# Kernel tuning notes

Measured on AMD Instinct MI355X. Metric: run time of the kernel, lower is better.

The kernel has to match this reference:

```python
import jax, jax.numpy as jnp
import numpy as np

N_NODES = 100000


def _gcn_conv(x, edge_index, W, b, num_nodes):
    """PyG GCNConv: x' = D^{-1/2} (A + I) D^{-1/2} (x W) + b."""
    xl = x @ W  # [N, H]
    loop = jnp.arange(num_nodes)
    row = jnp.concatenate([edge_index[0], loop])  # source
    col = jnp.concatenate([edge_index[1], loop])  # target
    deg = jax.ops.segment_sum(jnp.ones_like(col, dtype=xl.dtype), col,
                              num_segments=num_nodes)
    dinv = jnp.where(deg > 0, jax.lax.rsqrt(deg), 0.0)
    norm = dinv[row] * dinv[col]  # [E + N]
    msgs = xl[row] * norm[:, None]  # gather + scale
    out = jax.ops.segment_sum(msgs, col, num_segments=num_nodes)
    return out + b


def setup_inputs() -> dict:
    key = jax.random.key(0)
    ks = jax.random.split(key, 6)
    N, E, D, H, O = N_NODES, 1600000, 128, 64, 1
    x = jax.random.normal(ks[0], (N, D), dtype=jnp.float32)
    edge_index = jax.random.randint(ks[1], (2, E), 0, N, dtype=jnp.int64)
    W1 = jax.random.normal(ks[2], (D, H), dtype=jnp.float32) / np.sqrt(D)
    b1 = jnp.zeros((H,), dtype=jnp.float32)
    W2 = jax.random.normal(ks[3], (H, H), dtype=jnp.float32) / np.sqrt(H)
    b2 = jnp.zeros((H,), dtype=jnp.float32)
    Wfc = jax.random.normal(ks[4], (H, O), dtype=jnp.float32) / np.sqrt(H)
    bfc = jnp.zeros((O,), dtype=jnp.float32)
    return {"x": x, "edge_index": edge_index, "W1": W1, "b1": b1,
            "W2": W2, "b2": b2, "Wfc": Wfc, "bfc": bfc}


def reference(x, edge_index, W1, b1, W2, b2, Wfc, bfc):
    N = x.shape[0]
    h = jax.nn.relu(_gcn_conv(x, edge_index, W1, b1, N))
    h = jax.nn.relu(_gcn_conv(h, edge_index, W2, b2, N))
    return jax.nn.sigmoid(h @ Wfc + bfc)  # [N, 1]
```

## Files before the change

kernel.cpp:

```cpp
#include <hip/hip_runtime.h>
#include <math.h>


typedef __attribute__((ext_vector_type(8))) short bf16x8;
typedef __attribute__((ext_vector_type(4))) float f32x4;
typedef __attribute__((ext_vector_type(2))) float f32x2;

#define CHUNKS 1024

__device__ __forceinline__ unsigned short f2bf(float f) {
    unsigned u = __float_as_uint(f);
    u += 0x7FFFu + ((u >> 16) & 1u);
    return (unsigned short)(u >> 16);
}
__device__ __forceinline__ unsigned packbf(float a, float b) {
    return (unsigned)f2bf(a) | ((unsigned)f2bf(b) << 16);
}
__device__ __forceinline__ void upadd2(uint4 g, f32x2* a) {
    a[0] += (f32x2){__uint_as_float(g.x << 16), __uint_as_float(g.x & 0xFFFF0000u)};
    a[1] += (f32x2){__uint_as_float(g.y << 16), __uint_as_float(g.y & 0xFFFF0000u)};
    a[2] += (f32x2){__uint_as_float(g.z << 16), __uint_as_float(g.z & 0xFFFF0000u)};
    a[3] += (f32x2){__uint_as_float(g.w << 16), __uint_as_float(g.w & 0xFFFF0000u)};
}

__global__ __launch_bounds__(256) void k_hist(const int* __restrict__ col, int E,
                                              int NBUK, int CH,
                                              int* __restrict__ hist_g) {
    __shared__ int h[256];
    for (int i = threadIdx.x; i < NBUK; i += 256) h[i] = 0;
    __syncthreads();
    int base = blockIdx.x * CH, hi = min(base + CH, E);
    for (int e = base + (int)threadIdx.x; e < hi; e += 256)
        atomicAdd(&h[col[e] >> 9], 1);
    __syncthreads();
    for (int i = threadIdx.x; i < NBUK; i += 256)
        hist_g[blockIdx.x * NBUK + i] = h[i];
}

__global__ __launch_bounds__(256) void k_colscan(const int* __restrict__ hist_g, int NBUK,
                                                 int* __restrict__ histOff,
                                                 int* __restrict__ bucketTotal) {
    __shared__ int s[256];
    const int b = blockIdx.x, t = threadIdx.x;
    int v[4], sum = 0;
#pragma unroll
    for (int j = 0; j < 4; ++j) {
        v[j] = hist_g[(t * 4 + j) * NBUK + b];
        sum += v[j];
    }
    s[t] = sum;
    __syncthreads();
    for (int off = 1; off < 256; off <<= 1) {
        int u = (t >= off) ? s[t - off] : 0;
        __syncthreads();
        s[t] += u;
        __syncthreads();
    }
    int run = s[t] - sum;
#pragma unroll
    for (int j = 0; j < 4; ++j) {
        histOff[b * CHUNKS + t * 4 + j] = run;
        run += v[j];
    }
    if (t == 255) bucketTotal[b] = run;
}

__global__ __launch_bounds__(256) void k_scan_tot(const int* __restrict__ bucketTotal,
                                                  int NBUK, int E, int N,
                                                  int* __restrict__ bucketBase,
                                                  int* __restrict__ row_off) {
    __shared__ int s[256];
    int t = threadIdx.x;
    int v = (t < NBUK) ? bucketTotal[t] : 0;
    s[t] = v;
    __syncthreads();
    for (int off = 1; off < 256; off <<= 1) {
        int u = (t >= off) ? s[t - off] : 0;
        __syncthreads();
        s[t] += u;
        __syncthreads();
    }
    if (t < NBUK) bucketBase[t] = s[t] - v;
    if (t == 0) row_off[N] = E;
}

__global__ __launch_bounds__(256) void k_scatter(const int* __restrict__ row,
                                                 const int* __restrict__ col, int E,
                                                 int NBUK, int CH,
                                                 const int* __restrict__ bucketBase,
                                                 const int* __restrict__ histOff,
                                                 unsigned* __restrict__ ebuf) {
    __shared__ int cur[256];
    for (int i = threadIdx.x; i < NBUK; i += 256)
        cur[i] = bucketBase[i] + histOff[i * CHUNKS + blockIdx.x];
    __syncthreads();
    int base = blockIdx.x * CH, hi = min(base + CH, E);
    for (int e = base + (int)threadIdx.x; e < hi; e += 256) {
        int d = col[e], src = row[e];
        int b = d >> 9;
        int pos = atomicAdd(&cur[b], 1);
        ebuf[pos] = ((unsigned)(d & 511) << 17) | (unsigned)src;
    }
}

__global__ __launch_bounds__(512) void k_bucket(const unsigned* __restrict__ ebuf,
                                                const int* __restrict__ bucketBase,
                                                const int* __restrict__ bucketTotal,
                                                int N,
                                                int* __restrict__ row_off,
                                                float* __restrict__ dinv,
                                                int* __restrict__ csr_src) {
    __shared__ int hc[512], of[512];
    const int bid = blockIdx.x, t = threadIdx.x;
    const int base = bucketBase[bid];
    const int cnt  = bucketTotal[bid];
    hc[t] = 0;
    __syncthreads();
    for (int i = t; i < cnt; i += 512)
        atomicAdd(&hc[ebuf[base + i] >> 17], 1);
    __syncthreads();
    int v = hc[t];
    of[t] = v;
    __syncthreads();
    for (int off = 1; off < 512; off <<= 1) {
        int u = (t >= off) ? of[t - off] : 0;
        __syncthreads();
        of[t] += u;
        __syncthreads();
    }
    int excl = of[t] - v;
    int node = bid * 512 + t;
    if (node < N) {
        row_off[node] = base + excl;
        dinv[node] = rsqrtf((float)(v + 1));
    }
    of[t] = excl;
    __syncthreads();
    for (int i = t; i < cnt; i += 512) {
        unsigned e = ebuf[base + i];
        int dl = (int)(e >> 17), src = (int)(e & 0x1FFFFu);
        int pos = atomicAdd(&of[dl], 1);
        csr_src[base + pos] = src;
    }
}

template <int K, bool BF16IN>
__global__ __launch_bounds__(256) void k_gemm_mfma(const void* __restrict__ xin,
                                                   const float* __restrict__ W,
                                                   const float* __restrict__ dinv,
                                                   unsigned short* __restrict__ out,
                                                   int N) {
    constexpr int KS = K + 8;
    __shared__ short sX[64 * KS];
    __shared__ short sW[64 * KS];
    const int tid = threadIdx.x;
    const int wv = tid >> 6, lane = tid & 63;
    const int q = lane >> 4, m = lane & 15;
    const int nb = blockIdx.x * 64;

    for (int i = tid; i < K * 64; i += 256) {
        int k = i >> 6, c = i & 63;
        sW[c * KS + k] = (short)f2bf(W[i]);
    }
    if (BF16IN) {
        const unsigned short* xb = (const unsigned short*)xin;
        for (int i = tid; i < 64 * (K / 8); i += 256) {
            int r = i / (K / 8), c8 = (i % (K / 8)) * 8;
            int node = nb + r;
            uint4 v = make_uint4(0u, 0u, 0u, 0u);
            if (node < N) v = *(const uint4*)(xb + (size_t)node * K + c8);
            *(uint4*)(&sX[r * KS + c8]) = v;
        }
    } else {
        const float* xf = (const float*)xin;
        for (int i = tid; i < 64 * (K / 8); i += 256) {
            int r = i / (K / 8), c8 = (i % (K / 8)) * 8;
            int node = nb + r;
            uint4 v = make_uint4(0u, 0u, 0u, 0u);
            if (node < N) {
                float4 lo = *(const float4*)(xf + (size_t)node * K + c8);
                float4 hi = *(const float4*)(xf + (size_t)node * K + c8 + 4);
                v.x = packbf(lo.x, lo.y);
                v.y = packbf(lo.z, lo.w);
                v.z = packbf(hi.x, hi.y);
                v.w = packbf(hi.z, hi.w);
            }
            *(uint4*)(&sX[r * KS + c8]) = v;
        }
    }
    __syncthreads();

    f32x4 acc[4] = {};
    const short* aRow = &sX[(wv * 16 + m) * KS + q * 8];
#pragma unroll
    for (int k0 = 0; k0 < K; k0 += 32) {
        bf16x8 a = *(const bf16x8*)(aRow + k0);
#pragma unroll
        for (int ft = 0; ft < 4; ++ft) {
            bf16x8 b = *(const bf16x8*)(&sW[(ft * 16 + m) * KS + k0 + q * 8]);
            acc[ft] = __builtin_amdgcn_mfma_f32_16x16x32_bf16(a, b, acc[ft], 0, 0, 0);
        }
    }
#pragma unroll
    for (int r = 0; r < 4; ++r) {
        int node = nb + wv * 16 + q * 4 + r;
        if (node < N) {
            float di = dinv[node];
#pragma unroll
            for (int ft = 0; ft < 4; ++ft)
                out[(size_t)node * 64 + ft * 16 + m] = f2bf(acc[ft][r] * di);
        }
    }
}

__global__ __launch_bounds__(256) void k_agg_g2(const unsigned short* __restrict__ xl,
                                                const int* __restrict__ row_off,
                                                const int* __restrict__ csr_src,
                                                const float* __restrict__ dinv,
                                                const float* __restrict__ bias,
                                                const float* __restrict__ W2,
                                                unsigned short* __restrict__ out, int N) {
    constexpr int KS = 72;
    __shared__ short sH[4 * 16 * KS];
    __shared__ short sW2[64 * KS];
    const int tid = threadIdx.x;
    const int wv = tid >> 6, lane = tid & 63;
    const int s = lane >> 3, o = lane & 7;
    const int q = lane >> 4, m = lane & 15;

    for (int i = tid; i < 64 * 64; i += 256) {
        int k = i >> 6, n = i & 63;
        sW2[n * KS + k] = (short)f2bf(W2[i]);
    }
    short* myH = &sH[wv * 16 * KS];
    for (int i = lane; i < 8 * KS / 4; i += 64)
        ((unsigned long long*)(myH + 8 * KS))[i] = 0ull;
    __syncthreads();

    const int base8 = (blockIdx.x * 4 + wv) * 8;
    int node = base8 + s;
    const bool active = node < N;
    node = min(node, N - 1);
    const int beg = row_off[node];
    const int deg = row_off[node + 1] - beg;
    const int cnt = active ? deg + 1 : 0;
    int mx = cnt;
    mx = max(mx, __shfl_xor(mx, 8, 64));
    mx = max(mx, __shfl_xor(mx, 16, 64));
    mx = max(mx, __shfl_xor(mx, 32, 64));
    const char* xlb = (const char*)xl;
    const unsigned loff = (unsigned)(o << 4);
    f32x2 acc0[4] = {}, acc1[4] = {};
    int idx[4];
#pragma unroll
    for (int j = 0; j < 4; ++j) idx[j] = (j < deg) ? csr_src[beg + j] : node;
    for (int it = 0; it < mx; it += 4) {
        int c[4];
        bool v[4];
#pragma unroll
        for (int j = 0; j < 4; ++j) {
            c[j] = idx[j];
            v[j] = (it + j) < cnt;
            idx[j] = (it + 4 + j < deg) ? csr_src[beg + it + 4 + j] : node;
        }
        uint4 g0 = *(const uint4*)(xlb + (((unsigned)c[0] << 7) | loff));
        uint4 g1 = *(const uint4*)(xlb + (((unsigned)c[1] << 7) | loff));
        uint4 g2 = *(const uint4*)(xlb + (((unsigned)c[2] << 7) | loff));
        uint4 g3 = *(const uint4*)(xlb + (((unsigned)c[3] << 7) | loff));
        if (!v[0]) g0 = make_uint4(0u, 0u, 0u, 0u);
        if (!v[1]) g1 = make_uint4(0u, 0u, 0u, 0u);
        if (!v[2]) g2 = make_uint4(0u, 0u, 0u, 0u);
        if (!v[3]) g3 = make_uint4(0u, 0u, 0u, 0u);
        upadd2(g0, acc0);
        upadd2(g1, acc1);
        upadd2(g2, acc0);
        upadd2(g3, acc1);
    }
#pragma unroll
    for (int j = 0; j < 4; ++j) acc0[j] += acc1[j];
    {
        float di = dinv[node];
        float4 blo = *(const float4*)(bias + o * 8);
        float4 bhi = *(const float4*)(bias + o * 8 + 4);
        uint4 h;
        h.x = packbf(fmaxf(acc0[0].x * di + blo.x, 0.f), fmaxf(acc0[0].y * di + blo.y, 0.f));
        h.y = packbf(fmaxf(acc0[1].x * di + blo.z, 0.f), fmaxf(acc0[1].y * di + blo.w, 0.f));
        h.z = packbf(fmaxf(acc0[2].x * di + bhi.x, 0.f), fmaxf(acc0[2].y * di + bhi.y, 0.f));
        h.w = packbf(fmaxf(acc0[3].x * di + bhi.z, 0.f), fmaxf(acc0[3].y * di + bhi.w, 0.f));
        *(uint4*)(myH + s * KS + o * 8) = h;
    }
    f32x4 accm[4] = {};
#pragma unroll
    for (int k0 = 0; k0 < 64; k0 += 32) {
        bf16x8 a = *(const bf16x8*)(myH + m * KS + q * 8 + k0);
#pragma unroll
        for (int ft = 0; ft < 4; ++ft) {
            bf16x8 b = *(const bf16x8*)(&sW2[(ft * 16 + m) * KS + k0 + q * 8]);
            accm[ft] = __builtin_amdgcn_mfma_f32_16x16x32_bf16(a, b, accm[ft], 0, 0, 0);
        }
    }
    if (q < 2) {
#pragma unroll
        for (int r = 0; r < 4; ++r) {
            int node2 = base8 + q * 4 + r;
            if (node2 < N) {
                float di2 = dinv[node2];
#pragma unroll
                for (int ft = 0; ft < 4; ++ft)
                    out[(size_t)node2 * 64 + ft * 16 + m] = f2bf(accm[ft][r] * di2);
            }
        }
    }
}

__global__ __launch_bounds__(256) void k_agg_fc(const unsigned short* __restrict__ xl,
                                                const int* __restrict__ row_off,
                                                const int* __restrict__ csr_src,
                                                const float* __restrict__ dinv,
                                                const float* __restrict__ bias,
                                                const float* __restrict__ Wfc,
                                                const float* __restrict__ bfc,
                                                float* __restrict__ out, int N) {
    const int wave = threadIdx.x >> 6, lane = threadIdx.x & 63;
    const int s = lane >> 3, o = lane & 7;
    int node = (blockIdx.x * 4 + wave) * 8 + s;
    const bool active = node < N;
    node = min(node, N - 1);
    const int beg = row_off[node];
    const int deg = row_off[node + 1] - beg;
    const int cnt = active ? deg + 1 : 0;
    int mx = cnt;
    mx = max(mx, __shfl_xor(mx, 8, 64));
    mx = max(mx, __shfl_xor(mx, 16, 64));
    mx = max(mx, __shfl_xor(mx, 32, 64));
    const char* xlb = (const char*)xl;
    const unsigned loff = (unsigned)(o << 4);
    f32x2 acc0[4] = {}, acc1[4] = {};
    int idx[4];
#pragma unroll
    for (int j = 0; j < 4; ++j) idx[j] = (j < deg) ? csr_src[beg + j] : node;
    for (int it = 0; it < mx; it += 4) {
        int c[4];
        bool v[4];
#pragma unroll
        for (int j = 0; j < 4; ++j) {
            c[j] = idx[j];
            v[j] = (it + j) < cnt;
            idx[j] = (it + 4 + j < deg) ? csr_src[beg + it + 4 + j] : node;
        }
        uint4 g0 = *(const uint4*)(xlb + (((unsigned)c[0] << 7) | loff));
        uint4 g1 = *(const uint4*)(xlb + (((unsigned)c[1] << 7) | loff));
        uint4 g2 = *(const uint4*)(xlb + (((unsigned)c[2] << 7) | loff));
        uint4 g3 = *(const uint4*)(xlb + (((unsigned)c[3] << 7) | loff));
        if (!v[0]) g0 = make_uint4(0u, 0u, 0u, 0u);
        if (!v[1]) g1 = make_uint4(0u, 0u, 0u, 0u);
        if (!v[2]) g2 = make_uint4(0u, 0u, 0u, 0u);
        if (!v[3]) g3 = make_uint4(0u, 0u, 0u, 0u);
        upadd2(g0, acc0);
        upadd2(g1, acc1);
        upadd2(g2, acc0);
        upadd2(g3, acc1);
    }
#pragma unroll
    for (int j = 0; j < 4; ++j) acc0[j] += acc1[j];
    const float di = dinv[node];
    float4 blo = *(const float4*)(bias + o * 8);
    float4 bhi = *(const float4*)(bias + o * 8 + 4);
    float4 wlo = *(const float4*)(Wfc + o * 8);
    float4 whi = *(const float4*)(Wfc + o * 8 + 4);
    float v = 0.f;
    v += fmaxf(acc0[0].x * di + blo.x, 0.f) * wlo.x;
    v += fmaxf(acc0[0].y * di + blo.y, 0.f) * wlo.y;
    v += fmaxf(acc0[1].x * di + blo.z, 0.f) * wlo.z;
    v += fmaxf(acc0[1].y * di + blo.w, 0.f) * wlo.w;
    v += fmaxf(acc0[2].x * di + bhi.x, 0.f) * whi.x;
    v += fmaxf(acc0[2].y * di + bhi.y, 0.f) * whi.y;
    v += fmaxf(acc0[3].x * di + bhi.z, 0.f) * whi.z;
    v += fmaxf(acc0[3].y * di + bhi.w, 0.f) * whi.w;
    v += __shfl_xor(v, 1, 64);
    v += __shfl_xor(v, 2, 64);
    v += __shfl_xor(v, 4, 64);
    if (active && o == 0) out[node] = 1.f / (1.f + expf(-(v + bfc[0])));
}

extern "C" void kernel_launch(void* const* d_in, const int* in_sizes, int n_in,
                              void* d_out, int out_size, void* d_ws, size_t ws_size,
                              hipStream_t stream) {
    const float* x   = (const float*)d_in[0];
    const int*   ei  = (const int*)d_in[1];
    const float* W1  = (const float*)d_in[2];
    const float* b1  = (const float*)d_in[3];
    const float* W2  = (const float*)d_in[4];
    const float* b2  = (const float*)d_in[5];
    const float* Wfc = (const float*)d_in[6];
    const float* bfc = (const float*)d_in[7];
    float* out = (float*)d_out;

    const int H = in_sizes[3];
    const int D = in_sizes[2] / H;
    const int N = in_sizes[0] / D;
    const int E = in_sizes[1] / 2;
    const int* row = ei;
    const int* col = ei + E;
    const int NBUK = (N + 511) >> 9;
    const int CH   = (E + CHUNKS - 1) / CHUNKS;

    char* p = (char*)d_ws;
    auto carve = [&](size_t bytes) {
        char* r = p;
        p += (bytes + 255) & ~(size_t)255;
        return (void*)r;
    };
    int*            hist_g      = (int*)carve((size_t)CHUNKS * 256 * 4);
    int*            histOff     = (int*)carve((size_t)256 * CHUNKS * 4);
    int*            bucketTotal = (int*)carve((size_t)256 * 4);
    int*            bucketBase  = (int*)carve((size_t)256 * 4);
    unsigned*       ebuf        = (unsigned*)carve((size_t)E * 4);
    int*            csr_src     = (int*)carve((size_t)E * 4);
    int*            row_off     = (int*)carve((size_t)(N + 1) * 4);
    float*          dinv        = (float*)carve((size_t)N * 4);
    unsigned short* bufXL       = (unsigned short*)carve((size_t)N * 64 * 2);
    unsigned short* bufXL2      = (unsigned short*)carve((size_t)N * 64 * 2);
    (void)ws_size;

    const int TB = 256;
    k_hist<<<CHUNKS, TB, 0, stream>>>(col, E, NBUK, CH, hist_g);
    k_colscan<<<NBUK, TB, 0, stream>>>(hist_g, NBUK, histOff, bucketTotal);
    k_scan_tot<<<1, TB, 0, stream>>>(bucketTotal, NBUK, E, N, bucketBase, row_off);
    k_scatter<<<CHUNKS, TB, 0, stream>>>(row, col, E, NBUK, CH, bucketBase, histOff, ebuf);
    k_bucket<<<NBUK, 512, 0, stream>>>(ebuf, bucketBase, bucketTotal, N,
                                       row_off, dinv, csr_src);

    int gemmGrid = (N + 63) / 64;
    int aggGrid  = (N + 31) / 32;
    k_gemm_mfma<128, false><<<gemmGrid, TB, 0, stream>>>(x, W1, dinv, bufXL, N);
    k_agg_g2<<<aggGrid, TB, 0, stream>>>(bufXL, row_off, csr_src, dinv, b1, W2, bufXL2, N);
    k_agg_fc<<<aggGrid, TB, 0, stream>>>(bufXL2, row_off, csr_src, dinv, b2, Wfc, bfc, out, N);
}
```

Baseline: 215.7 us.

## Use edge-balanced merge-path aggregation with packed CSR and LDS atomics

The CSR entries now keep the packed local destination index alongside the source index. Each aggregation block covers 64 nodes and splits that block's whole edge range evenly across 32 thread slots, instead of giving one lane-group per node and looping to the wave's maximum degree. Partial sums are flushed into a shared-memory accumulator with atomics whenever the destination changes. The self-loop term is added during a separate epilogue pass. This removes per-wave load imbalance from the skewed degree distribution, at the cost of LDS float atomics, extra barriers, and a single-edge serial loop per thread with a two-deep prefetch.

Measured after the change: 287.3 us. 1.33x slower.

```diff
diff --git a/kernel.cpp b/kernel.cpp
--- a/kernel.cpp
+++ b/kernel.cpp
@@ -138,9 +138,9 @@
     __syncthreads();
     for (int i = t; i < cnt; i += 512) {
         unsigned e = ebuf[base + i];
-        int dl = (int)(e >> 17), src = (int)(e & 0x1FFFFu);
+        int dl = (int)(e >> 17);
         int pos = atomicAdd(&of[dl], 1);
-        csr_src[base + pos] = src;
+        csr_src[base + pos] = (int)e;
     }
 }
 
@@ -215,172 +215,222 @@
 
 __global__ __launch_bounds__(256) void k_agg_g2(const unsigned short* __restrict__ xl,
                                                 const int* __restrict__ row_off,
-                                                const int* __restrict__ csr_src,
+                                                const int* __restrict__ csr,
                                                 const float* __restrict__ dinv,
                                                 const float* __restrict__ bias,
                                                 const float* __restrict__ W2,
                                                 unsigned short* __restrict__ out, int N) {
+    constexpr int PAD = 65;
     constexpr int KS = 72;
-    __shared__ short sH[4 * 16 * KS];
+    __shared__ float sAcc[64 * PAD];
+    __shared__ short sH[64 * KS];
     __shared__ short sW2[64 * KS];
     const int tid = threadIdx.x;
     const int wv = tid >> 6, lane = tid & 63;
-    const int s = lane >> 3, o = lane & 7;
+    const int slot = tid >> 3, o = tid & 7;
     const int q = lane >> 4, m = lane & 15;
+    const int nb = blockIdx.x * 64;
 
     for (int i = tid; i < 64 * 64; i += 256) {
         int k = i >> 6, n = i & 63;
         sW2[n * KS + k] = (short)f2bf(W2[i]);
     }
-    short* myH = &sH[wv * 16 * KS];
-    for (int i = lane; i < 8 * KS / 4; i += 64)
-        ((unsigned long long*)(myH + 8 * KS))[i] = 0ull;
-    __syncthreads();
-
-    const int base8 = (blockIdx.x * 4 + wv) * 8;
-    int node = base8 + s;
-    const bool active = node < N;
-    node = min(node, N - 1);
-    const int beg = row_off[node];
-    const int deg = row_off[node + 1] - beg;
-    const int cnt = active ? deg + 1 : 0;
-    int mx = cnt;
-    mx = max(mx, __shfl_xor(mx, 8, 64));
-    mx = max(mx, __shfl_xor(mx, 16, 64));
-    mx = max(mx, __shfl_xor(mx, 32, 64));
+    for (int i = tid; i < 2080; i += 256)
+        ((unsigned long long*)sAcc)[i] = 0ull;
+    __syncthreads();
+
+    const int nend = min(nb + 64, N);
+    const int beg = row_off[nb];
+    const int end = row_off[nend];
+    const int blocal = nb & 511;
     const char* xlb = (const char*)xl;
     const unsigned loff = (unsigned)(o << 4);
-    f32x2 acc0[4] = {}, acc1[4] = {};
-    int idx[4];
-#pragma unroll
-    for (int j = 0; j < 4; ++j) idx[j] = (j < deg) ? csr_src[beg + j] : node;
-    for (int it = 0; it < mx; it += 4) {
-        int c[4];
-        bool v[4];
-#pragma unroll
-        for (int j = 0; j < 4; ++j) {
-            c[j] = idx[j];
-            v[j] = (it + j) < cnt;
-            idx[j] = (it + 4 + j < deg) ? csr_src[beg + it + 4 + j] : node;
-        }
-        uint4 g0 = *(const uint4*)(xlb + (((unsigned)c[0] << 7) | loff));
-        uint4 g1 = *(const uint4*)(xlb + (((unsigned)c[1] << 7) | loff));
-        uint4 g2 = *(const uint4*)(xlb + (((unsigned)c[2] << 7) | loff));
-        uint4 g3 = *(const uint4*)(xlb + (((unsigned)c[3] << 7) | loff));
-        if (!v[0]) g0 = make_uint4(0u, 0u, 0u, 0u);
-        if (!v[1]) g1 = make_uint4(0u, 0u, 0u, 0u);
-        if (!v[2]) g2 = make_uint4(0u, 0u, 0u, 0u);
-        if (!v[3]) g3 = make_uint4(0u, 0u, 0u, 0u);
-        upadd2(g0, acc0);
-        upadd2(g1, acc1);
-        upadd2(g2, acc0);
-        upadd2(g3, acc1);
-    }
-#pragma unroll
-    for (int j = 0; j < 4; ++j) acc0[j] += acc1[j];
-    {
-        float di = dinv[node];
-        float4 blo = *(const float4*)(bias + o * 8);
-        float4 bhi = *(const float4*)(bias + o * 8 + 4);
-        uint4 h;
-        h.x = packbf(fmaxf(acc0[0].x * di + blo.x, 0.f), fmaxf(acc0[0].y * di + blo.y, 0.f));
-        h.y = packbf(fmaxf(acc0[1].x * di + blo.z, 0.f), fmaxf(acc0[1].y * di + blo.w, 0.f));
-        h.z = packbf(fmaxf(acc0[2].x * di + bhi.x, 0.f), fmaxf(acc0[2].y * di + bhi.y, 0.f));
-        h.w = packbf(fmaxf(acc0[3].x * di + bhi.z, 0.f), fmaxf(acc0[3].y * di + bhi.w, 0.f));
-        *(uint4*)(myH + s * KS + o * 8) = h;
-    }
+
+    const int span = end - beg;
+    const int len = (span + 31) >> 5;
+    int e0 = beg + slot * len;
+    int e1 = min(e0 + len, end);
+    f32x2 a0[4] = {};
+    int cur = -1;
+    if (e0 < e1) {
+        int pk0 = csr[e0];
+        int pk1 = csr[(e0 + 1 < e1) ? e0 + 1 : e1 - 1];
+        uint4 G0 = *(const uint4*)(xlb + (((unsigned)(pk0 & 0x1FFFF) << 7) | loff));
+        uint4 G1 = *(const uint4*)(xlb + (((unsigned)(pk1 & 0x1FFFF) << 7) | loff));
+        for (int e = e0; e < e1; ++e) {
+            int pk2 = csr[(e + 2 < e1) ? e + 2 : e1 - 1];
+            uint4 G2 = *(const uint4*)(xlb + (((unsigned)(pk2 & 0x1FFFF) << 7) | loff));
+            int li = (pk0 >> 17) - blocal;
+            if (li != cur) {
+                if (cur >= 0) {
+                    float* dst = &sAcc[cur * PAD + o * 8];
+                    atomicAdd(dst + 0, a0[0].x); atomicAdd(dst + 1, a0[0].y);
+                    atomicAdd(dst + 2, a0[1].x); atomicAdd(dst + 3, a0[1].y);
+                    atomicAdd(dst + 4, a0[2].x); atomicAdd(dst + 5, a0[2].y);
+                    atomicAdd(dst + 6, a0[3].x); atomicAdd(dst + 7, a0[3].y);
+                }
+                a0[0] = (f32x2){0.f, 0.f}; a0[1] = (f32x2){0.f, 0.f};
+                a0[2] = (f32x2){0.f, 0.f}; a0[3] = (f32x2){0.f, 0.f};
+                cur = li;
+            }
+            upadd2(G0, a0);
+            pk0 = pk1; pk1 = pk2; G0 = G1; G1 = G2;
+        }
+        if (cur >= 0) {
+            float* dst = &sAcc[cur * PAD + o * 8];
+            atomicAdd(dst + 0, a0[0].x); atomicAdd(dst + 1, a0[0].y);
+            atomicAdd(dst + 2, a0[1].x); atomicAdd(dst + 3, a0[1].y);
+            atomicAdd(dst + 4, a0[2].x); atomicAdd(dst + 5, a0[2].y);
+            atomicAdd(dst + 6, a0[3].x); atomicAdd(dst + 7, a0[3].y);
+        }
+    }
+    __syncthreads();
+
+    for (int i = lane; i < 128; i += 64) {
+        int row = i >> 3, oo = i & 7;
+        int li = wv * 16 + row;
+        int node = nb + li;
+        int cn = min(node, N - 1);
+        uint4 ow = *(const uint4*)(xl + (size_t)cn * 64 + oo * 8);
+        f32x2 own[4] = {};
+        upadd2(ow, own);
+        float di = dinv[cn];
+        const float* ap = &sAcc[li * PAD + oo * 8];
+        float4 blo = *(const float4*)(bias + oo * 8);
+        float4 bhi = *(const float4*)(bias + oo * 8 + 4);
+        float h0 = fmaxf((ap[0] + own[0].x) * di + blo.x, 0.f);
+        float h1 = fmaxf((ap[1] + own[0].y) * di + blo.y, 0.f);
+        float h2 = fmaxf((ap[2] + own[1].x) * di + blo.z, 0.f);
+        float h3 = fmaxf((ap[3] + own[1].y) * di + blo.w, 0.f);
+        float h4 = fmaxf((ap[4] + own[2].x) * di + bhi.x, 0.f);
+        float h5 = fmaxf((ap[5] + own[2].y) * di + bhi.y, 0.f);
+        float h6 = fmaxf((ap[6] + own[3].x) * di + bhi.z, 0.f);
+        float h7 = fmaxf((ap[7] + own[3].y) * di + bhi.w, 0.f);
+        uint4 hq = make_uint4(0u, 0u, 0u, 0u);
+        if (node < N) {
+            hq.x = packbf(h0, h1); hq.y = packbf(h2, h3);
+            hq.z = packbf(h4, h5); hq.w = packbf(h6, h7);
+        }
+        *(uint4*)(&sH[li * KS + oo * 8]) = hq;
+    }
+    __syncthreads();
+
     f32x4 accm[4] = {};
+    const short* aRow = &sH[(wv * 16 + m) * KS + q * 8];
 #pragma unroll
     for (int k0 = 0; k0 < 64; k0 += 32) {
-        bf16x8 a = *(const bf16x8*)(myH + m * KS + q * 8 + k0);
+        bf16x8 aa = *(const bf16x8*)(aRow + k0);
 #pragma unroll
         for (int ft = 0; ft < 4; ++ft) {
-            bf16x8 b = *(const bf16x8*)(&sW2[(ft * 16 + m) * KS + k0 + q * 8]);
-            accm[ft] = __builtin_amdgcn_mfma_f32_16x16x32_bf16(a, b, accm[ft], 0, 0, 0);
-        }
-    }
-    if (q < 2) {
-#pragma unroll
-        for (int r = 0; r < 4; ++r) {
-            int node2 = base8 + q * 4 + r;
-            if (node2 < N) {
-                float di2 = dinv[node2];
-#pragma unroll
-                for (int ft = 0; ft < 4; ++ft)
-                    out[(size_t)node2 * 64 + ft * 16 + m] = f2bf(accm[ft][r] * di2);
-            }
+            bf16x8 bb = *(const bf16x8*)(&sW2[(ft * 16 + m) * KS + k0 + q * 8]);
+            accm[ft] = __builtin_amdgcn_mfma_f32_16x16x32_bf16(aa, bb, accm[ft], 0, 0, 0);
+        }
+    }
+#pragma unroll
+    for (int r = 0; r < 4; ++r) {
+        int node2 = nb + wv * 16 + q * 4 + r;
+        if (node2 < N) {
+            float di2 = dinv[node2];
+#pragma unroll
+            for (int ft = 0; ft < 4; ++ft)
+                out[(size_t)node2 * 64 + ft * 16 + m] = f2bf(accm[ft][r] * di2);
         }
     }
 }
 
 __global__ __launch_bounds__(256) void k_agg_fc(const unsigned short* __restrict__ xl,
                                                 const int* __restrict__ row_off,
-                                                const int* __restrict__ csr_src,
+                                                const int* __restrict__ csr,
                                                 const float* __restrict__ dinv,
                                                 const float* __restrict__ bias,
                                                 const float* __restrict__ Wfc,
                                                 const float* __restrict__ bfc,
                                                 float* __restrict__ out, int N) {
-    const int wave = threadIdx.x >> 6, lane = threadIdx.x & 63;
-    const int s = lane >> 3, o = lane & 7;
-    int node = (blockIdx.x * 4 + wave) * 8 + s;
-    const bool active = node < N;
-    node = min(node, N - 1);
-    const int beg = row_off[node];
-    const int deg = row_off[node + 1] - beg;
-    const int cnt = active ? deg + 1 : 0;
-    int mx = cnt;
-    mx = max(mx, __shfl_xor(mx, 8, 64));
-    mx = max(mx, __shfl_xor(mx, 16, 64));
-    mx = max(mx, __shfl_xor(mx, 32, 64));
+    constexpr int PAD = 65;
+    __shared__ float sAcc[64 * PAD];
+    const int tid = threadIdx.x;
+    const int slot = tid >> 3, o = tid & 7;
+    const int nb = blockIdx.x * 64;
+
+    for (int i = tid; i < 2080; i += 256)
+        ((unsigned long long*)sAcc)[i] = 0ull;
+    __syncthreads();
+
+    const int nend = min(nb + 64, N);
+    const int beg = row_off[nb];
+    const int end = row_off[nend];
+    const int blocal = nb & 511;
     const char* xlb = (const char*)xl;
     const unsigned loff = (unsigned)(o << 4);
-    f32x2 acc0[4] = {}, acc1[4] = {};
-    int idx[4];
-#pragma unroll
-    for (int j = 0; j < 4; ++j) idx[j] = (j < deg) ? csr_src[beg + j] : node;
-    for (int it = 0; it < mx; it += 4) {
-        int c[4];
-        bool v[4];
-#pragma unroll
-        for (int j = 0; j < 4; ++j) {
-            c[j] = idx[j];
-            v[j] = (it + j) < cnt;
-            idx[j] = (it + 4 + j < deg) ? csr_src[beg + it + 4 + j] : node;
-        }
-        uint4 g0 = *(const uint4*)(xlb + (((unsigned)c[0] << 7) | loff));
-        uint4 g1 = *(const uint4*)(xlb + (((unsigned)c[1] << 7) | loff));
-        uint4 g2 = *(const uint4*)(xlb + (((unsigned)c[2] << 7) | loff));
-        uint4 g3 = *(const uint4*)(xlb + (((unsigned)c[3] << 7) | loff));
-        if (!v[0]) g0 = make_uint4(0u, 0u, 0u, 0u);
-        if (!v[1]) g1 = make_uint4(0u, 0u, 0u, 0u);
-        if (!v[2]) g2 = make_uint4(0u, 0u, 0u, 0u);
-        if (!v[3]) g3 = make_uint4(0u, 0u, 0u, 0u);
-        upadd2(g0, acc0);
-        upadd2(g1, acc1);
-        upadd2(g2, acc0);
-        upadd2(g3, acc1);
-    }
-#pragma unroll
-    for (int j = 0; j < 4; ++j) acc0[j] += acc1[j];
-    const float di = dinv[node];
-    float4 blo = *(const float4*)(bias + o * 8);
-    float4 bhi = *(const float4*)(bias + o * 8 + 4);
-    float4 wlo = *(const float4*)(Wfc + o * 8);
-    float4 whi = *(const float4*)(Wfc + o * 8 + 4);
-    float v = 0.f;
-    v += fmaxf(acc0[0].x * di + blo.x, 0.f) * wlo.x;
-    v += fmaxf(acc0[0].y * di + blo.y, 0.f) * wlo.y;
-    v += fmaxf(acc0[1].x * di + blo.z, 0.f) * wlo.z;
-    v += fmaxf(acc0[1].y * di + blo.w, 0.f) * wlo.w;
-    v += fmaxf(acc0[2].x * di + bhi.x, 0.f) * whi.x;
-    v += fmaxf(acc0[2].y * di + bhi.y, 0.f) * whi.y;
-    v += fmaxf(acc0[3].x * di + bhi.z, 0.f) * whi.z;
-    v += fmaxf(acc0[3].y * di + bhi.w, 0.f) * whi.w;
-    v += __shfl_xor(v, 1, 64);
-    v += __shfl_xor(v, 2, 64);
-    v += __shfl_xor(v, 4, 64);
-    if (active && o == 0) out[node] = 1.f / (1.f + expf(-(v + bfc[0])));
+
+    const int span = end - beg;
+    const int len = (span + 31) >> 5;
+    int e0 = beg + slot * len;
+    int e1 = min(e0 + len, end);
+    f32x2 a0[4] = {};
+    int cur = -1;
+    if (e0 < e1) {
+        int pk0 = csr[e0];
+        int pk1 = csr[(e0 + 1 < e1) ? e0 + 1 : e1 - 1];
+        uint4 G0 = *(const uint4*)(xlb + (((unsigned)(pk0 & 0x1FFFF) << 7) | loff));
+        uint4 G1 = *(const uint4*)(xlb + (((unsigned)(pk1 & 0x1FFFF) << 7) | loff));
+        for (int e = e0; e < e1; ++e) {
+            int pk2 = csr[(e + 2 < e1) ? e + 2 : e1 - 1];
+            uint4 G2 = *(const uint4*)(xlb + (((unsigned)(pk2 & 0x1FFFF) << 7) | loff));
+            int li = (pk0 >> 17) - blocal;
+            if (li != cur) {
+                if (cur >= 0) {
+                    float* dst = &sAcc[cur * PAD + o * 8];
+                    atomicAdd(dst + 0, a0[0].x); atomicAdd(dst + 1, a0[0].y);
+                    atomicAdd(dst + 2, a0[1].x); atomicAdd(dst + 3, a0[1].y);
+                    atomicAdd(dst + 4, a0[2].x); atomicAdd(dst + 5, a0[2].y);
+                    atomicAdd(dst + 6, a0[3].x); atomicAdd(dst + 7, a0[3].y);
+                }
+                a0[0] = (f32x2){0.f, 0.f}; a0[1] = (f32x2){0.f, 0.f};
+                a0[2] = (f32x2){0.f, 0.f}; a0[3] = (f32x2){0.f, 0.f};
+                cur = li;
+            }
+            upadd2(G0, a0);
+            pk0 = pk1; pk1 = pk2; G0 = G1; G1 = G2;
+        }
+        if (cur >= 0) {
+            float* dst = &sAcc[cur * PAD + o * 8];
+            atomicAdd(dst + 0, a0[0].x); atomicAdd(dst + 1, a0[0].y);
+            atomicAdd(dst + 2, a0[1].x); atomicAdd(dst + 3, a0[1].y);
+            atomicAdd(dst + 4, a0[2].x); atomicAdd(dst + 5, a0[2].y);
+            atomicAdd(dst + 6, a0[3].x); atomicAdd(dst + 7, a0[3].y);
+        }
+    }
+    __syncthreads();
+
+    for (int i = tid; i < 512; i += 256) {
+        int row = i >> 3, oo = i & 7;
+        int node = nb + row;
+        int cn = min(node, N - 1);
+        uint4 ow = *(const uint4*)(xl + (size_t)cn * 64 + oo * 8);
+        f32x2 own[4] = {};
+        upadd2(ow, own);
+        float di = dinv[cn];
+        const float* ap = &sAcc[row * PAD + oo * 8];
+        float4 blo = *(const float4*)(bias + oo * 8);
+        float4 bhi = *(const float4*)(bias + oo * 8 + 4);
+        float4 wlo = *(const float4*)(Wfc + oo * 8);
+        float4 whi = *(const float4*)(Wfc + oo * 8 + 4);
+        float v = 0.f;
+        v += fmaxf((ap[0] + own[0].x) * di + blo.x, 0.f) * wlo.x;
+        v += fmaxf((ap[1] + own[0].y) * di + blo.y, 0.f) * wlo.y;
+        v += fmaxf((ap[2] + own[1].x) * di + blo.z, 0.f) * wlo.z;
+        v += fmaxf((ap[3] + own[1].y) * di + blo.w, 0.f) * wlo.w;
+        v += fmaxf((ap[4] + own[2].x) * di + bhi.x, 0.f) * whi.x;
+        v += fmaxf((ap[5] + own[2].y) * di + bhi.y, 0.f) * whi.y;
+        v += fmaxf((ap[6] + own[3].x) * di + bhi.z, 0.f) * whi.z;
+        v += fmaxf((ap[7] + own[3].y) * di + bhi.w, 0.f) * whi.w;
+        v += __shfl_xor(v, 1, 64);
+        v += __shfl_xor(v, 2, 64);
+        v += __shfl_xor(v, 4, 64);
+        if (node < N && oo == 0)
+            out[node] = 1.f / (1.f + expf(-(v + bfc[0])));
+    }
 }
 
 extern "C" void kernel_launch(void* const* d_in, const int* in_sizes, int n_in,
@@ -432,7 +482,7 @@
                                        row_off, dinv, csr_src);
 
     int gemmGrid = (N + 63) / 64;
-    int aggGrid  = (N + 31) / 32;
+    int aggGrid  = (N + 63) / 64;
     k_gemm_mfma<128, false><<<gemmGrid, TB, 0, stream>>>(x, W1, dinv, bufXL, N);
     k_agg_g2<<<aggGrid, TB, 0, stream>>>(bufXL, row_off, csr_src, dinv, b1, W2, bufXL2, N);
     k_agg_fc<<<aggGrid, TB, 0, stream>>>(bufXL2, row_off, csr_src, dinv, b2, Wfc, bfc, out, N);
```

## Sort nodes by degree so aggregation waves process similar-degree nodes

Applied to the files above, without the earlier changes.

Adds a counting sort of nodes by in-degree (histogram, scan, scatter kernels) to produce a permutation, largest degree first. Both aggregation kernels then map the 8 nodes of each wave slot through this permutation, so nodes grouped in a wave have similar degree and less loop divergence from the max-degree wait. The cost is three extra small kernel launches and an extra indirection, plus loss of node locality for output writes and gathers.

Result: slower. 272.6 us (+26.4%).

```diff
diff --git a/kernel.cpp b/kernel.cpp
--- a/kernel.cpp
+++ b/kernel.cpp
@@ -7,6 +7,7 @@
 typedef __attribute__((ext_vector_type(2))) float f32x2;
 
 #define CHUNKS 1024
+#define DBINS 256
 
 __device__ __forceinline__ unsigned short f2bf(float f) {
     unsigned u = __float_as_uint(f);
@@ -141,6 +142,59 @@
         int dl = (int)(e >> 17), src = (int)(e & 0x1FFFFu);
         int pos = atomicAdd(&of[dl], 1);
         csr_src[base + pos] = src;
+    }
+}
+
+__global__ __launch_bounds__(256) void k_deg_hist(const int* __restrict__ row_off, int N,
+                                                  int* __restrict__ dhist) {
+    __shared__ int h[DBINS];
+    for (int i = threadIdx.x; i < DBINS; i += 256) h[i] = 0;
+    __syncthreads();
+    int base = blockIdx.x * 512, lim = min(base + 512, N);
+    for (int i = base + (int)threadIdx.x; i < lim; i += 256) {
+        int deg = row_off[i + 1] - row_off[i];
+        int bin = 255 - min(deg, 255);
+        atomicAdd(&h[bin], 1);
+    }
+    __syncthreads();
+    for (int i = threadIdx.x; i < DBINS; i += 256)
+        dhist[blockIdx.x * DBINS + i] = h[i];
+}
+
+__global__ __launch_bounds__(256) void k_deg_scan(const int* __restrict__ dhist, int NB,
+                                                  int* __restrict__ dOff) {
+    __shared__ int s[256];
+    const int b = threadIdx.x;
+    int tot = 0;
+    for (int c = 0; c < NB; ++c) tot += dhist[c * DBINS + b];
+    s[b] = tot;
+    __syncthreads();
+    for (int off = 1; off < 256; off <<= 1) {
+        int u = (b >= off) ? s[b - off] : 0;
+        __syncthreads();
+        s[b] += u;
+        __syncthreads();
+    }
+    int run = s[b] - tot;
+    for (int c = 0; c < NB; ++c) {
+        dOff[c * DBINS + b] = run;
+        run += dhist[c * DBINS + b];
+    }
+}
+
+__global__ __launch_bounds__(256) void k_deg_scatter(const int* __restrict__ row_off, int N,
+                                                     const int* __restrict__ dOff,
+                                                     int* __restrict__ perm) {
+    __shared__ int cur[DBINS];
+    for (int i = threadIdx.x; i < DBINS; i += 256)
+        cur[i] = dOff[blockIdx.x * DBINS + i];
+    __syncthreads();
+    int base = blockIdx.x * 512, lim = min(base + 512, N);
+    for (int i = base + (int)threadIdx.x; i < lim; i += 256) {
+        int deg = row_off[i + 1] - row_off[i];
+        int bin = 255 - min(deg, 255);
+        int pos = atomicAdd(&cur[bin], 1);
+        perm[pos] = i;
     }
 }
 
@@ -219,6 +273,7 @@
                                                 const float* __restrict__ dinv,
                                                 const float* __restrict__ bias,
                                                 const float* __restrict__ W2,
+                                                const int* __restrict__ perm,
                                                 unsigned short* __restrict__ out, int N) {
     constexpr int KS = 72;
     __shared__ short sH[4 * 16 * KS];
@@ -238,9 +293,9 @@
     __syncthreads();
 
     const int base8 = (blockIdx.x * 4 + wv) * 8;
-    int node = base8 + s;
-    const bool active = node < N;
-    node = min(node, N - 1);
+    const int gi = base8 + s;
+    const bool active = gi < N;
+    const int node = perm[min(gi, N - 1)];
     const int beg = row_off[node];
     const int deg = row_off[node + 1] - beg;
     const int cnt = active ? deg + 1 : 0;
@@ -302,8 +357,9 @@
     if (q < 2) {
 #pragma unroll
         for (int r = 0; r < 4; ++r) {
-            int node2 = base8 + q * 4 + r;
-            if (node2 < N) {
+            int gi2 = base8 + q * 4 + r;
+            if (gi2 < N) {
+                int node2 = perm[gi2];
                 float di2 = dinv[node2];
 #pragma unroll
                 for (int ft = 0; ft < 4; ++ft)
@@ -320,12 +376,13 @@
                                                 const float* __restrict__ bias,
                                                 const float* __restrict__ Wfc,
                                                 const float* __restrict__ bfc,
+                                                const int* __restrict__ perm,
                                                 float* __restrict__ out, int N) {
     const int wave = threadIdx.x >> 6, lane = threadIdx.x & 63;
     const int s = lane >> 3, o = lane & 7;
-    int node = (blockIdx.x * 4 + wave) * 8 + s;
-    const bool active = node < N;
-    node = min(node, N - 1);
+    const int gi = (blockIdx.x * 4 + wave) * 8 + s;
+    const bool active = gi < N;
+    const int node = perm[min(gi, N - 1)];
     const int beg = row_off[node];
     const int deg = row_off[node + 1] - beg;
     const int cnt = active ? deg + 1 : 0;
@@ -419,6 +476,9 @@
     int*            csr_src     = (int*)carve((size_t)E * 4);
     int*            row_off     = (int*)carve((size_t)(N + 1) * 4);
     float*          dinv        = (float*)carve((size_t)N * 4);
+    int*            perm        = (int*)carve((size_t)N * 4);
+    int*            dhist       = (int*)carve((size_t)NBUK * DBINS * 4);
+    int*            dOff        = (int*)carve((size_t)NBUK * DBINS * 4);
     unsigned short* bufXL       = (unsigned short*)carve((size_t)N * 64 * 2);
     unsigned short* bufXL2      = (unsigned short*)carve((size_t)N * 64 * 2);
     (void)ws_size;
@@ -430,10 +490,13 @@
     k_scatter<<<CHUNKS, TB, 0, stream>>>(row, col, E, NBUK, CH, bucketBase, histOff, ebuf);
     k_bucket<<<NBUK, 512, 0, stream>>>(ebuf, bucketBase, bucketTotal, N,
                                        row_off, dinv, csr_src);
+    k_deg_hist<<<NBUK, TB, 0, stream>>>(row_off, N, dhist);
+    k_deg_scan<<<1, TB, 0, stream>>>(dhist, NBUK, dOff);
+    k_deg_scatter<<<NBUK, TB, 0, stream>>>(row_off, N, dOff, perm);
 
     int gemmGrid = (N + 63) / 64;
     int aggGrid  = (N + 31) / 32;
     k_gemm_mfma<128, false><<<gemmGrid, TB, 0, stream>>>(x, W1, dinv, bufXL, N);
-    k_agg_g2<<<aggGrid, TB, 0, stream>>>(bufXL, row_off, csr_src, dinv, b1, W2, bufXL2, N);
-    k_agg_fc<<<aggGrid, TB, 0, stream>>>(bufXL2, row_off, csr_src, dinv, b2, Wfc, bfc, out, N);
-}
+    k_agg_g2<<<aggGrid, TB, 0, stream>>>(bufXL, row_off, csr_src, dinv, b1, W2, perm, bufXL2, N);
+    k_agg_fc<<<aggGrid, TB, 0, stream>>>(bufXL2, row_off, csr_src, dinv, b2, Wfc, bfc, perm, out, N);
+}
```
